# Optimization experiments

Hardware: AMD Instinct MI355X
Metric: run time of the kernel (lower is better)

## Reference

```python
import jax, jax.numpy as jnp
import numpy as np

DIM = 384
HEADS = 12
WS = 7
MLPH = 1536
B = 32
EPS = 1e-5


def _rel_index():
    coords = np.stack(np.meshgrid(np.arange(WS), np.arange(WS), indexing='ij'))  # [2,7,7]
    cf = coords.reshape(2, -1)  # [2,49]
    rel = cf[:, :, None] - cf[:, None, :]  # [2,49,49]
    rel = rel.transpose(1, 2, 0).astype(np.int64)
    rel[:, :, 0] += WS - 1
    rel[:, :, 1] += WS - 1
    rel[:, :, 0] *= 2 * WS - 1
    return jnp.asarray(rel.sum(-1), dtype=jnp.int32)  # [49,49]


def setup_inputs() -> dict:
    key = jax.random.key(0)
    ks = jax.random.split(key, 16)
    H, W = 56, 56
    L = H * W
    s = 0.02
    inp = {
        'x': jax.random.normal(ks[0], (B, L, DIM), jnp.float32),
        'ln1_g': jnp.ones((DIM,), jnp.float32),
        'ln1_b': jnp.zeros((DIM,), jnp.float32),
        'qkv_w': jax.random.normal(ks[1], (DIM, 3 * DIM), jnp.float32) * s,
        'qkv_b': jnp.zeros((3 * DIM,), jnp.float32),
        'rpb_table': jax.random.normal(ks[2], ((2 * WS - 1) ** 2, HEADS), jnp.float32) * s,
        'proj_w': jax.random.normal(ks[3], (DIM, DIM), jnp.float32) * s,
        'proj_b': jnp.zeros((DIM,), jnp.float32),
        'ln2_g': jnp.ones((DIM,), jnp.float32),
        'ln2_b': jnp.zeros((DIM,), jnp.float32),
        'mlp_w1': jax.random.normal(ks[4], (DIM, MLPH), jnp.float32) * s,
        'mlp_b1': jnp.zeros((MLPH,), jnp.float32),
        'mlp_w2': jax.random.normal(ks[5], (MLPH, DIM), jnp.float32) * s,
        'mlp_b2': jnp.zeros((DIM,), jnp.float32),
        'rel_idx': _rel_index(),
        'H': H,
        'W': W,
    }
    return inp


def _ln(x, g, b):
    m = jnp.mean(x, axis=-1, keepdims=True)
    v = jnp.mean(jnp.square(x - m), axis=-1, keepdims=True)
    return (x - m) * jax.lax.rsqrt(v + EPS) * g + b


def reference(x, ln1_g, ln1_b, qkv_w, qkv_b, rpb_table, proj_w, proj_b,
              ln2_g, ln2_b, mlp_w1, mlp_b1, mlp_w2, mlp_b2, rel_idx, H, W):
    Bb, L, C = x.shape
    N = WS * WS
    hd = C // HEADS
    scale = hd ** -0.5

    shortcut = x
    h = _ln(x, ln1_g, ln1_b).reshape(Bb, H, W, C)
    # window partition -> [nW, 49, C]
    h = h.reshape(Bb, H // WS, WS, W // WS, WS, C).transpose(0, 1, 3, 2, 4, 5)
    wins = h.reshape(-1, N, C)
    nW = wins.shape[0]

    qkv = (wins @ qkv_w + qkv_b).reshape(nW, N, 3, HEADS, hd).transpose(2, 0, 3, 1, 4)
    q, k, v = qkv[0] * scale, qkv[1], qkv[2]  # [nW, heads, 49, hd]

    attn = jnp.einsum('bhnd,bhmd->bhnm', q, k)
    bias = rpb_table[rel_idx].transpose(2, 0, 1)  # [heads,49,49]
    attn = jax.nn.softmax(attn + bias[None], axis=-1)
    out = jnp.einsum('bhnm,bhmd->bhnd', attn, v).transpose(0, 2, 1, 3).reshape(nW, N, C)
    out = out @ proj_w + proj_b

    # window reverse -> [B, L, C]
    out = out.reshape(Bb, H // WS, W // WS, WS, WS, C).transpose(0, 1, 3, 2, 4, 5).reshape(Bb, L, C)

    x = shortcut + out
    h2 = _ln(x, ln2_g, ln2_b)
    mlp = jax.nn.gelu(h2 @ mlp_w1 + mlp_b1, approximate=False) @ mlp_w2 + mlp_b2
    return x + mlp
```

## Files before the change

### kernel.cpp

```cpp
#include <hip/hip_runtime.h>
#include <hip/hip_bf16.h>
#include <cstdint>
#include <cstddef>

#define HEADS 12
#define LL 3136
#define ROWS 100352
#define SCALE 0.17677669529663687f

typedef __hip_bfloat16 bf16;
typedef __attribute__((ext_vector_type(8))) short short8;
typedef __attribute__((ext_vector_type(4))) short s4;
typedef __attribute__((ext_vector_type(4))) float f32x4;

__device__ __forceinline__ float bf2f(unsigned short u) {
  union { uint32_t u32; float f; } x; x.u32 = ((uint32_t)u) << 16; return x.f;
}
__device__ __forceinline__ unsigned short f2bf_bits(float f) {
  union { float f; uint32_t u; } x; x.f = f;
  uint32_t r = x.u + 0x7fffu + ((x.u >> 16) & 1u);
  return (unsigned short)(r >> 16);
}

__global__ __launch_bounds__(64) void prep_fragB(const float* __restrict__ src,
    bf16* __restrict__ dst, int K, int N, int scaleLim, float scale) {
  const int nf = blockIdx.x, kf = blockIdx.y;
  const int l = threadIdx.x;
  const int n = nf * 16 + (l & 15);
  const int k0 = kf * 32 + (l >> 4) * 8;
  const float sc = (n < scaleLim) ? scale : 1.f;
  short8 v;
  #pragma unroll
  for (int j = 0; j < 8; ++j)
    v[j] = (short)f2bf_bits(src[(size_t)(k0 + j) * N + n] * sc);
  *(short8*)&dst[(((size_t)nf * (K >> 5) + kf) * 64 + l) * 8] = v;
}

__global__ void prep_qb(const float* __restrict__ qkv_b, float* __restrict__ qb) {
  int idx = blockIdx.x * 256 + threadIdx.x;
  if (idx < 1152) qb[idx] = qkv_b[idx] * (idx < 384 ? SCALE : 1.0f);
}

__global__ void prep_biasM(const float* __restrict__ rpb, const int* __restrict__ rel,
                           f32x4* __restrict__ biasM) {
  int h = blockIdx.x;
  int t = blockIdx.y;
  int mi = t >> 2, ni = t & 3;
  int lane = threadIdx.x;
  int q = ni * 16 + (lane & 15);
  int g = lane >> 4;
  f32x4 v;
  #pragma unroll
  for (int j = 0; j < 4; ++j) {
    int k = mi * 16 + g * 4 + j;
    float b;
    if (k < 49) b = (q < 49) ? rpb[rel[q * 49 + k] * HEADS + h] : 0.f;
    else        b = -1e30f;
    v[j] = b;
  }
  biasM[((h * 4 + mi) * 4 + ni) * 64 + lane] = v;
}

template<bool WIN>
__global__ __launch_bounds__(256) void ln_kernel(const float* __restrict__ x,
    const float* __restrict__ g, const float* __restrict__ b, bf16* __restrict__ out) {
  int row = blockIdx.x * 4 + (threadIdx.x >> 6);
  int lane = threadIdx.x & 63;
  size_t src;
  if (WIN) {
    int w = row / 49, p = row - w * 49;
    int bb = w >> 6, wy = (w >> 3) & 7, wx = w & 7;
    int iy = p / 7, ix = p - iy * 7;
    int l = (wy * 7 + iy) * 56 + wx * 7 + ix;
    src = ((size_t)bb * LL + l) * 384;
  } else {
    src = (size_t)row * 384;
  }
  const float* xr = x + src;
  float vals[6];
  float s = 0.f, s2 = 0.f;
  #pragma unroll
  for (int j = 0; j < 6; ++j) {
    float v = xr[lane + 64 * j];
    vals[j] = v; s += v; s2 += v * v;
  }
  #pragma unroll
  for (int off = 32; off >= 1; off >>= 1) {
    s  += __shfl_xor(s, off);
    s2 += __shfl_xor(s2, off);
  }
  float m  = s * (1.f / 384.f);
  float var = s2 * (1.f / 384.f) - m * m;
  float rs = rsqrtf(var + 1e-5f);
  bf16* orow = out + (size_t)row * 384;
  #pragma unroll
  for (int j = 0; j < 6; ++j) {
    int c = lane + 64 * j;
    orow[c] = __float2bfloat16((vals[j] - m) * rs * g[c] + b[c]);
  }
}

template<int EPI>
__global__ __launch_bounds__(256) void gemm_bt(const bf16* __restrict__ A,
    const bf16* __restrict__ Bt, const float* __restrict__ bias,
    bf16* __restrict__ Cb, float* __restrict__ Cf, const float* __restrict__ resid,
    int M, int N, int K) {
  __shared__ bf16 lsA[2][128 * 32];
  const int t = threadIdx.x;
  const int lane = t & 63;
  const int wave = t >> 6;
  const int wm = wave >> 1, wn = wave & 1;
  const int lrow = lane & 15;
  const int lk = (lane >> 4) * 8;
  const int nbx = N >> 7;
  const int nwg = (M >> 7) * nbx;
  const int cpx = nwg >> 3;
  const int id2 = (blockIdx.x & 7) * cpx + (blockIdx.x >> 3);
  const int n0 = (id2 % nbx) * 128;
  const int m0 = (id2 / nbx) * 128;
  const int nkf = K >> 5;

  f32x4 acc[4][4];
  #pragma unroll
  for (int i = 0; i < 4; ++i)
    #pragma unroll
    for (int j = 0; j < 4; ++j) acc[i][j] = (f32x4){0.f, 0.f, 0.f, 0.f};

  auto stageA = [&](int buf, int tile) {
    int k0 = tile * 32;
    #pragma unroll
    for (int i = 0; i < 2; ++i) {
      int e = (i * 256 + t) * 8;
      int r = e >> 5, c = e & 31;
      const bf16* ga = A + (size_t)(m0 + r) * K + (k0 + c);
      __builtin_amdgcn_global_load_lds((const __attribute__((address_space(1))) void*)ga,
          (__attribute__((address_space(3))) void*)&lsA[buf][e], 16, 0, 0);
    }
  };

  auto loadB = [&](int kf, short8* dst) {
    const bf16* fb = Bt + (((size_t)((n0 >> 4) + wn * 4) * nkf + kf) * 64 + lane) * 8;
    #pragma unroll
    for (int ni = 0; ni < 4; ++ni)
      dst[ni] = *(const short8*)(fb + (size_t)ni * nkf * 512);
  };

  auto computeA = [&](int buf, const short8* bfr) {
    short8 af[4];
    #pragma unroll
    for (int mi = 0; mi < 4; ++mi)
      af[mi] = *(const short8*)&lsA[buf][(wm * 64 + mi * 16 + lrow) * 32 + lk];
    #pragma unroll
    for (int mi = 0; mi < 4; ++mi)
      #pragma unroll
      for (int ni = 0; ni < 4; ++ni)
        acc[mi][ni] = __builtin_amdgcn_mfma_f32_16x16x32_bf16(af[mi], bfr[ni], acc[mi][ni], 0, 0, 0);
  };

  const int nt = K >> 5;
  short8 b0[4], b1[4];
  stageA(0, 0);
  loadB(0, b0);
  __syncthreads();
  int cur = 0;
  for (int it = 0; it < nt; ++it) {
    if (it + 1 < nt) {
      stageA(cur ^ 1, it + 1);
      loadB(it + 1, b1);
    }
    computeA(cur, b0);
    __syncthreads();
    if (it + 1 < nt) {
      #pragma unroll
      for (int i = 0; i < 4; ++i) b0[i] = b1[i];
    }
    cur ^= 1;
  }

  #pragma unroll
  for (int mi = 0; mi < 4; ++mi) {
    #pragma unroll
    for (int ni = 0; ni < 4; ++ni) {
      int col = n0 + wn * 64 + ni * 16 + lrow;
      float bv = bias[col];
      #pragma unroll
      for (int j = 0; j < 4; ++j) {
        int row = m0 + wm * 64 + mi * 16 + (lane >> 4) * 4 + j;
        float v = acc[mi][ni][j] + bv;
        if constexpr (EPI == 0) {
          Cb[(size_t)row * N + col] = __float2bfloat16(v);
        } else if constexpr (EPI == 1) {
          v = v * 0.5f * (1.0f + erff(v * 0.70710678118654752f));
          Cb[(size_t)row * N + col] = __float2bfloat16(v);
        } else if constexpr (EPI == 2) {
          int w = row / 49, p = row - w * 49;
          int bb = w >> 6, wy = (w >> 3) & 7, wx = w & 7;
          int iy = p / 7, ix = p - iy * 7;
          int l = (wy * 7 + iy) * 56 + wx * 7 + ix;
          size_t di = ((size_t)bb * LL + l) * 384 + col;
          Cf[di] = v + resid[di];
        } else {
          size_t di = (size_t)row * N + col;
          Cf[di] = v + resid[di];
        }
      }
    }
  }
}

__global__ __launch_bounds__(256) void attn_mfma(const bf16* __restrict__ qkv,
    const f32x4* __restrict__ biasM, bf16* __restrict__ out) {
  __shared__ __align__(16) short lds4[4][6272];
  const int wv = threadIdx.x >> 6;
  const int lane = threadIdx.x & 63;
  const int w = blockIdx.x * 4 + wv;
  const int h = blockIdx.y;
  short* L = &lds4[wv][0];
  const short* base = (const short*)(qkv + (size_t)w * 49 * 1152 + h * 32);

  #pragma unroll
  for (int i = 0; i < 4; ++i) {
    int t = i * 64 + lane;
    int r = t >> 2, c = t & 3;
    short8 qv, kv, vv;
    if (r < 49) {
      const short* rp = base + (size_t)r * 1152;
      qv = *(const short8*)(rp + c * 8);
      kv = *(const short8*)(rp + 384 + c * 8);
      vv = *(const short8*)(rp + 768 + c * 8);
    } else {
      qv = (short8)0; kv = (short8)0; vv = (short8)0;
    }
    *(short8*)&L[r * 32 + c * 8] = kv;
    *(short8*)&L[2048 + r * 32 + c * 8] = qv;
    #pragma unroll
    for (int j = 0; j < 8; ++j) L[4096 + (c * 8 + j) * 68 + r] = vv[j];
  }

  const int g = lane >> 4, r15 = lane & 15;

  short8 ka[4], qb[4];
  #pragma unroll
  for (int mi = 0; mi < 4; ++mi)
    ka[mi] = *(const short8*)&L[(mi * 16 + r15) * 32 + g * 8];
  #pragma unroll
  for (int ni = 0; ni < 4; ++ni)
    qb[ni] = *(const short8*)&L[2048 + (ni * 16 + r15) * 32 + g * 8];

  f32x4 sT[4][4];
  #pragma unroll
  for (int mi = 0; mi < 4; ++mi)
    #pragma unroll
    for (int ni = 0; ni < 4; ++ni)
      sT[mi][ni] = biasM[((h * 4 + mi) * 4 + ni) * 64 + lane];
  #pragma unroll
  for (int mi = 0; mi < 4; ++mi)
    #pragma unroll
    for (int ni = 0; ni < 4; ++ni)
      sT[mi][ni] = __builtin_amdgcn_mfma_f32_16x16x32_bf16(ka[mi], qb[ni], sT[mi][ni], 0, 0, 0);

  float inv_[4];
  #pragma unroll
  for (int ni = 0; ni < 4; ++ni) {
    float m = -1e30f;
    #pragma unroll
    for (int mi = 0; mi < 4; ++mi)
      #pragma unroll
      for (int j = 0; j < 4; ++j) m = fmaxf(m, sT[mi][ni][j]);
    m = fmaxf(m, __shfl_xor(m, 16));
    m = fmaxf(m, __shfl_xor(m, 32));
    float s = 0.f;
    #pragma unroll
    for (int mi = 0; mi < 4; ++mi)
      #pragma unroll
      for (int j = 0; j < 4; ++j) {
        float p = __expf(sT[mi][ni][j] - m);
        sT[mi][ni][j] = p; s += p;
      }
    s += __shfl_xor(s, 16);
    s += __shfl_xor(s, 32);
    inv_[ni] = 1.f / s;
  }

  s4 pa[4][4];
  #pragma unroll
  for (int mi = 0; mi < 4; ++mi)
    #pragma unroll
    for (int ni = 0; ni < 4; ++ni) {
      s4 p;
      #pragma unroll
      for (int j = 0; j < 4; ++j)
        p[j] = (short)f2bf_bits(sT[mi][ni][j] * inv_[ni]);
      pa[mi][ni] = p;
    }

  s4 vb[4][2];
  #pragma unroll
  for (int mi = 0; mi < 4; ++mi)
    #pragma unroll
    for (int di = 0; di < 2; ++di)
      vb[mi][di] = *(const s4*)&L[4096 + (di * 16 + r15) * 68 + mi * 16 + g * 4];

  f32x4 o[4][2];
  #pragma unroll
  for (int ni = 0; ni < 4; ++ni)
    #pragma unroll
    for (int di = 0; di < 2; ++di) o[ni][di] = (f32x4){0.f, 0.f, 0.f, 0.f};

  asm volatile("s_nop 3" ::: );
  #pragma unroll
  for (int ni = 0; ni < 4; ++ni)
    #pragma unroll
    for (int di = 0; di < 2; ++di)
      #pragma unroll
      for (int mi = 0; mi < 4; ++mi) {
#if __has_builtin(__builtin_amdgcn_mfma_f32_16x16x16bf16_1k)
        o[ni][di] = __builtin_amdgcn_mfma_f32_16x16x16bf16_1k(pa[mi][ni], vb[mi][di], o[ni][di], 0, 0, 0);
#else
        asm volatile("v_mfma_f32_16x16x16_bf16 %0, %1, %2, %0"
                     : "+v"(o[ni][di]) : "v"(pa[mi][ni]), "v"(vb[mi][di]));
#endif
      }
  asm volatile("s_nop 7\n\ts_nop 7" ::: );

  bf16* op = out + ((size_t)w * 49) * 384 + h * 32;
  #pragma unroll
  for (int ni = 0; ni < 4; ++ni)
    #pragma unroll
    for (int di = 0; di < 2; ++di)
      #pragma unroll
      for (int j = 0; j < 4; ++j) {
        int q = ni * 16 + g * 4 + j;
        if (q < 49)
          op[(size_t)q * 384 + di * 16 + r15] = __float2bfloat16(o[ni][di][j]);
      }
}

extern "C" void kernel_launch(void* const* d_in, const int* in_sizes, int n_in,
                              void* d_out, int out_size, void* d_ws, size_t ws_size,
                              hipStream_t stream) {
  const float* x      = (const float*)d_in[0];
  const float* ln1_g  = (const float*)d_in[1];
  const float* ln1_b  = (const float*)d_in[2];
  const float* qkv_w  = (const float*)d_in[3];
  const float* qkv_b  = (const float*)d_in[4];
  const float* rpb    = (const float*)d_in[5];
  const float* proj_w = (const float*)d_in[6];
  const float* proj_b = (const float*)d_in[7];
  const float* ln2_g  = (const float*)d_in[8];
  const float* ln2_b  = (const float*)d_in[9];
  const float* mlp_w1 = (const float*)d_in[10];
  const float* mlp_b1 = (const float*)d_in[11];
  const float* mlp_w2 = (const float*)d_in[12];
  const float* mlp_b2 = (const float*)d_in[13];
  const int*   rel    = (const int*)d_in[14];

  char* ws = (char*)d_ws;
  const size_t OFF_WQKV  = 0;
  const size_t OFF_WPROJ = OFF_WQKV + (size_t)1152 * 384 * 2;
  const size_t OFF_WM1   = OFF_WPROJ + (size_t)384 * 384 * 2;
  const size_t OFF_WM2   = OFF_WM1 + (size_t)1536 * 384 * 2;
  const size_t OFF_QB    = OFF_WM2 + (size_t)384 * 1536 * 2;
  const size_t OFF_HWIN  = 3659776;
  const size_t OFF_QKV   = OFF_HWIN + (size_t)ROWS * 384 * 2;
  const size_t OFF_ATTN  = OFF_QKV + (size_t)ROWS * 1152 * 2;
  const size_t OFF_X2    = OFF_ATTN + (size_t)ROWS * 384 * 2;
  const size_t OFF_M1    = OFF_QKV;
  const size_t OFF_H2    = OFF_HWIN;
  const size_t OFF_BIASM = OFF_X2;

  bf16*  wqkv  = (bf16*)(ws + OFF_WQKV);
  bf16*  wproj = (bf16*)(ws + OFF_WPROJ);
  bf16*  wm1   = (bf16*)(ws + OFF_WM1);
  bf16*  wm2   = (bf16*)(ws + OFF_WM2);
  float* qb    = (float*)(ws + OFF_QB);
  f32x4* biasM = (f32x4*)(ws + OFF_BIASM);
  bf16*  hwin  = (bf16*)(ws + OFF_HWIN);
  bf16*  qkvb  = (bf16*)(ws + OFF_QKV);
  bf16*  attnb = (bf16*)(ws + OFF_ATTN);
  float* x2    = (float*)(ws + OFF_X2);
  bf16*  m1    = (bf16*)(ws + OFF_M1);
  bf16*  h2    = (bf16*)(ws + OFF_H2);
  float* outp  = (float*)d_out;

  prep_fragB<<<dim3(1152 / 16, 384 / 32), 64, 0, stream>>>(qkv_w, wqkv, 384, 1152, 384, SCALE);
  prep_fragB<<<dim3(384 / 16, 384 / 32), 64, 0, stream>>>(proj_w, wproj, 384, 384, 0, 1.f);
  prep_fragB<<<dim3(1536 / 16, 384 / 32), 64, 0, stream>>>(mlp_w1, wm1, 384, 1536, 0, 1.f);
  prep_fragB<<<dim3(384 / 16, 1536 / 32), 64, 0, stream>>>(mlp_w2, wm2, 1536, 384, 0, 1.f);
  prep_qb<<<5, 256, 0, stream>>>(qkv_b, qb);
  prep_biasM<<<dim3(12, 16), 64, 0, stream>>>(rpb, rel, biasM);

  ln_kernel<true><<<ROWS / 4, 256, 0, stream>>>(x, ln1_g, ln1_b, hwin);
  gemm_bt<0><<<(1152 / 128) * (ROWS / 128), 256, 0, stream>>>(
      hwin, wqkv, qb, qkvb, nullptr, nullptr, ROWS, 1152, 384);
  attn_mfma<<<dim3(512, HEADS), 256, 0, stream>>>(qkvb, biasM, attnb);
  gemm_bt<2><<<(384 / 128) * (ROWS / 128), 256, 0, stream>>>(
      attnb, wproj, proj_b, nullptr, x2, x, ROWS, 384, 384);
  ln_kernel<false><<<ROWS / 4, 256, 0, stream>>>(x2, ln2_g, ln2_b, h2);
  gemm_bt<1><<<(1536 / 128) * (ROWS / 128), 256, 0, stream>>>(
      h2, wm1, mlp_b1, m1, nullptr, nullptr, ROWS, 1536, 384);
  gemm_bt<3><<<(384 / 128) * (ROWS / 128), 256, 0, stream>>>(
      m1, wm2, mlp_b2, nullptr, outp, x2, ROWS, 384, 1536);
}
```

Baseline: 939.7 us.

## Triple-buffer GEMM A tiles with explicit waitcnt, store residual stream in bf16

The GEMM main loop moves from a double-buffered LDS scheme with __syncthreads to a three-stage ring. It issues prefetch two tiles ahead, uses manual s_waitcnt vmcnt counts and raw barriers, and raises wave priority around the MFMA block. Separately, the intermediate residual x2 is now written and read as bf16 instead of fp32 by the proj epilogue, LN2 and the final residual add, which roughly halves that traffic. The bf16 residual loses precision in the skip path, and the hand-coded vmcnt values are fragile if the compiler reorders loads.

```diff
diff --git a/kernel.cpp b/kernel.cpp
--- a/kernel.cpp
+++ b/kernel.cpp
@@ -61,9 +61,10 @@
   biasM[((h * 4 + mi) * 4 + ni) * 64 + lane] = v;
 }
 
-template<bool WIN>
-__global__ __launch_bounds__(256) void ln_kernel(const float* __restrict__ x,
-    const float* __restrict__ g, const float* __restrict__ b, bf16* __restrict__ out) {
+template<bool WIN, bool BF16IN>
+__global__ __launch_bounds__(256) void ln_kernel(const float* __restrict__ xf,
+    const bf16* __restrict__ xb, const float* __restrict__ g,
+    const float* __restrict__ b, bf16* __restrict__ out) {
   int row = blockIdx.x * 4 + (threadIdx.x >> 6);
   int lane = threadIdx.x & 63;
   size_t src;
@@ -76,12 +77,12 @@
   } else {
     src = (size_t)row * 384;
   }
-  const float* xr = x + src;
   float vals[6];
   float s = 0.f, s2 = 0.f;
   #pragma unroll
   for (int j = 0; j < 6; ++j) {
-    float v = xr[lane + 64 * j];
+    float v = BF16IN ? bf2f(*(const unsigned short*)&xb[src + lane + 64 * j])
+                     : xf[src + lane + 64 * j];
     vals[j] = v; s += v; s2 += v * v;
   }
   #pragma unroll
@@ -104,8 +105,8 @@
 __global__ __launch_bounds__(256) void gemm_bt(const bf16* __restrict__ A,
     const bf16* __restrict__ Bt, const float* __restrict__ bias,
     bf16* __restrict__ Cb, float* __restrict__ Cf, const float* __restrict__ resid,
-    int M, int N, int K) {
-  __shared__ bf16 lsA[2][128 * 32];
+    const bf16* __restrict__ residb, int M, int N, int K) {
+  __shared__ bf16 lsA[3][128 * 32];
   const int t = threadIdx.x;
   const int lane = t & 63;
   const int wave = t >> 6;
@@ -138,43 +139,58 @@
     }
   };
 
-  auto loadB = [&](int kf, short8* dst) {
+  auto loadB = [&](int kf, short8 (&dst)[4]) {
     const bf16* fb = Bt + (((size_t)((n0 >> 4) + wn * 4) * nkf + kf) * 64 + lane) * 8;
     #pragma unroll
     for (int ni = 0; ni < 4; ++ni)
       dst[ni] = *(const short8*)(fb + (size_t)ni * nkf * 512);
   };
 
-  auto computeA = [&](int buf, const short8* bfr) {
+  auto computeA = [&](int buf, const short8 (&bfr)[4]) {
     short8 af[4];
     #pragma unroll
     for (int mi = 0; mi < 4; ++mi)
       af[mi] = *(const short8*)&lsA[buf][(wm * 64 + mi * 16 + lrow) * 32 + lk];
+    __builtin_amdgcn_s_setprio(1);
     #pragma unroll
     for (int mi = 0; mi < 4; ++mi)
       #pragma unroll
       for (int ni = 0; ni < 4; ++ni)
         acc[mi][ni] = __builtin_amdgcn_mfma_f32_16x16x32_bf16(af[mi], bfr[ni], acc[mi][ni], 0, 0, 0);
+    __builtin_amdgcn_s_setprio(0);
   };
 
   const int nt = K >> 5;
   short8 b0[4], b1[4];
   stageA(0, 0);
   loadB(0, b0);
-  __syncthreads();
+  stageA(1, 1);
   int cur = 0;
-  for (int it = 0; it < nt; ++it) {
+  for (int it = 0; it < nt; it += 2) {
+    {
+      __builtin_amdgcn_s_barrier();
+      if (it + 1 < nt) loadB(it + 1, b1);
+      if (it + 2 < nt) stageA((cur + 2) % 3, it + 2);
+      int rem = nt - 1 - it;
+      if (rem >= 2)      asm volatile("s_waitcnt vmcnt(12)" ::: "memory");
+      else if (rem == 1) asm volatile("s_waitcnt vmcnt(10)" ::: "memory");
+      else               asm volatile("s_waitcnt vmcnt(4)"  ::: "memory");
+      __builtin_amdgcn_s_barrier();
+      computeA(cur, b0);
+      cur = (cur == 2) ? 0 : cur + 1;
+    }
     if (it + 1 < nt) {
-      stageA(cur ^ 1, it + 1);
-      loadB(it + 1, b1);
-    }
-    computeA(cur, b0);
-    __syncthreads();
-    if (it + 1 < nt) {
-      #pragma unroll
-      for (int i = 0; i < 4; ++i) b0[i] = b1[i];
-    }
-    cur ^= 1;
+      __builtin_amdgcn_s_barrier();
+      if (it + 2 < nt) loadB(it + 2, b0);
+      if (it + 3 < nt) stageA((cur + 2) % 3, it + 3);
+      int rem = nt - 2 - it;
+      if (rem >= 2)      asm volatile("s_waitcnt vmcnt(12)" ::: "memory");
+      else if (rem == 1) asm volatile("s_waitcnt vmcnt(10)" ::: "memory");
+      else               asm volatile("s_waitcnt vmcnt(4)"  ::: "memory");
+      __builtin_amdgcn_s_barrier();
+      computeA(cur, b1);
+      cur = (cur == 2) ? 0 : cur + 1;
+    }
   }
 
   #pragma unroll
@@ -198,10 +214,10 @@
           int iy = p / 7, ix = p - iy * 7;
           int l = (wy * 7 + iy) * 56 + wx * 7 + ix;
           size_t di = ((size_t)bb * LL + l) * 384 + col;
-          Cf[di] = v + resid[di];
+          Cb[di] = __float2bfloat16(v + resid[di]);
         } else {
           size_t di = (size_t)row * N + col;
-          Cf[di] = v + resid[di];
+          Cf[di] = v + bf2f(*(const unsigned short*)&residb[di]);
         }
       }
     }
@@ -367,7 +383,7 @@
   const size_t OFF_X2    = OFF_ATTN + (size_t)ROWS * 384 * 2;
   const size_t OFF_M1    = OFF_QKV;
   const size_t OFF_H2    = OFF_HWIN;
-  const size_t OFF_BIASM = OFF_X2;
+  const size_t OFF_BIASM = OFF_X2 + (size_t)ROWS * 384 * 2;
 
   bf16*  wqkv  = (bf16*)(ws + OFF_WQKV);
   bf16*  wproj = (bf16*)(ws + OFF_WPROJ);
@@ -378,7 +394,7 @@
   bf16*  hwin  = (bf16*)(ws + OFF_HWIN);
   bf16*  qkvb  = (bf16*)(ws + OFF_QKV);
   bf16*  attnb = (bf16*)(ws + OFF_ATTN);
-  float* x2    = (float*)(ws + OFF_X2);
+  bf16*  x2b   = (bf16*)(ws + OFF_X2);
   bf16*  m1    = (bf16*)(ws + OFF_M1);
   bf16*  h2    = (bf16*)(ws + OFF_H2);
   float* outp  = (float*)d_out;
@@ -390,15 +406,15 @@
   prep_qb<<<5, 256, 0, stream>>>(qkv_b, qb);
   prep_biasM<<<dim3(12, 16), 64, 0, stream>>>(rpb, rel, biasM);
 
-  ln_kernel<true><<<ROWS / 4, 256, 0, stream>>>(x, ln1_g, ln1_b, hwin);
+  ln_kernel<true, false><<<ROWS / 4, 256, 0, stream>>>(x, nullptr, ln1_g, ln1_b, hwin);
   gemm_bt<0><<<(1152 / 128) * (ROWS / 128), 256, 0, stream>>>(
-      hwin, wqkv, qb, qkvb, nullptr, nullptr, ROWS, 1152, 384);
+      hwin, wqkv, qb, qkvb, nullptr, nullptr, nullptr, ROWS, 1152, 384);
   attn_mfma<<<dim3(512, HEADS), 256, 0, stream>>>(qkvb, biasM, attnb);
   gemm_bt<2><<<(384 / 128) * (ROWS / 128), 256, 0, stream>>>(
-      attnb, wproj, proj_b, nullptr, x2, x, ROWS, 384, 384);
-  ln_kernel<false><<<ROWS / 4, 256, 0, stream>>>(x2, ln2_g, ln2_b, h2);
+      attnb, wproj, proj_b, x2b, nullptr, x, nullptr, ROWS, 384, 384);
+  ln_kernel<false, true><<<ROWS / 4, 256, 0, stream>>>(nullptr, x2b, ln2_g, ln2_b, h2);
   gemm_bt<1><<<(1536 / 128) * (ROWS / 128), 256, 0, stream>>>(
-      h2, wm1, mlp_b1, m1, nullptr, nullptr, ROWS, 1536, 384);
+      h2, wm1, mlp_b1, m1, nullptr, nullptr, nullptr, ROWS, 1536, 384);
   gemm_bt<3><<<(384 / 128) * (ROWS / 128), 256, 0, stream>>>(
-      m1, wm2, mlp_b2, nullptr, outp, x2, ROWS, 384, 1536);
-}
+      m1, wm2, mlp_b2, nullptr, outp, nullptr, x2b, ROWS, 384, 1536);
+}
```

Result: slower. 972.3 us (+3.5%).
